# Kernel optimization log

Hardware: AMD Instinct MI355X
Metric: run time of the kernel (lower is better)

The kernel has to match this reference:

```python
import jax, jax.numpy as jnp
import numpy as np

D_MODEL = 1024
D_INNER = 4096
K = 127
B, L = 2, 4096

def setup_inputs() -> dict:
    key = jax.random.key(0)
    k1, k2, k3, k4, k5 = jax.random.split(key, 5)
    x = jax.random.normal(k1, (B, L, D_MODEL), dtype=jnp.float32)
    # in_proj: Linear(d, 2*m) -> weight [2m, d] (torch convention)
    w_in = jax.random.normal(k2, (2 * D_INNER, D_MODEL), dtype=jnp.float32) * (1.0 / np.sqrt(D_MODEL))
    # depthwise conv weight: [m, 1, k] in torch; store as [m, k]
    w_dw = jax.random.normal(k3, (D_INNER, K), dtype=jnp.float32) * (1.0 / np.sqrt(K))
    b_dw = jax.random.normal(k4, (D_INNER,), dtype=jnp.float32) * 0.01
    # out_proj: Linear(m, d) -> weight [d, m]
    w_out = jax.random.normal(k5, (D_MODEL, D_INNER), dtype=jnp.float32) * (1.0 / np.sqrt(D_INNER))
    return {"x": x, "w_in": w_in, "w_dw": w_dw, "b_dw": b_dw, "w_out": w_out}

def _causal_dwconv(v, w_dw, b_dw):
    # v: [B, L, m]; causal depthwise conv with kernel K
    # pad K-1 on the left only (equivalent to torch pad=K-1 then [..., :L])
    v_bcl = jnp.transpose(v, (0, 2, 1))  # [B, m, L]
    out = jax.lax.conv_general_dilated(
        v_bcl,
        w_dw[:, None, :],  # [m, 1, K]
        window_strides=(1,),
        padding=[(K - 1, 0)],
        feature_group_count=D_INNER,
        dimension_numbers=("NCH", "OIH", "NCH"),
    )
    out = out + b_dw[None, :, None]
    return jnp.transpose(out, (0, 2, 1))  # [B, L, m]

def reference(x, w_in, w_dw, b_dw, w_out):
    vg = jnp.einsum("bld,ed->ble", x, w_in)  # [B, L, 2m]
    v, g = jnp.split(vg, 2, axis=-1)
    v = _causal_dwconv(v, w_dw, b_dw)
    y = jax.nn.silu(v) * jax.nn.silu(g)
    return jnp.einsum("blm,dm->bld", y, w_out)
```

## Files before the change

kernel.cpp:

```cpp
#include <hip/hip_runtime.h>
#include <hip/hip_bf16.h>
#include <cstdint>
#include <cstddef>

typedef __fp16 f16_t;
typedef __attribute__((ext_vector_type(8))) __fp16 f16x8;
typedef __attribute__((ext_vector_type(4))) __fp16 f16x4;
typedef __attribute__((ext_vector_type(2))) __fp16 h2_t;
typedef __attribute__((ext_vector_type(4))) float floatx4;

__device__ __forceinline__ void async_copy_16B(const void* g, void* l) {
  __builtin_amdgcn_global_load_lds(
      (const __attribute__((address_space(1))) void*)g,
      (__attribute__((address_space(3))) void*)l, 16, 0, 0);
}

__global__ __launch_bounds__(256) void prep(
    const float* __restrict__ x, const float* __restrict__ w_in,
    const float* __restrict__ w_out, const float* __restrict__ w_dw,
    f16_t* __restrict__ x_h, f16_t* __restrict__ wi_h,
    f16_t* __restrict__ wo_h, h2_t* __restrict__ wp) {
  const int tid = blockIdx.x * 256 + threadIdx.x;
  if (tid < 5242880) {
    const float* src;
    f16_t* dst;
    int off;
    if (tid < 2097152) {
      src = x; dst = x_h; off = tid;
    } else if (tid < 4194304) {
      src = w_in; dst = wi_h; off = tid - 2097152;
    } else {
      src = w_out; dst = wo_h; off = tid - 4194304;
    }
    const float4 v = *(const float4*)(src + (size_t)off * 4);
    f16x4 o;
    o.x = (f16_t)v.x; o.y = (f16_t)v.y; o.z = (f16_t)v.z; o.w = (f16_t)v.w;
    *(f16x4*)(dst + (size_t)off * 4) = o;
  } else {
    const int idx = tid - 5242880;
    if (idx < 128 * 4096) {
      const int p = idx >> 12;
      const int c = idx & 4095;
      float a, b;
      if (p < 126) {
        a = w_dw[c * 127 + p]; b = w_dw[c * 127 + p + 1];
      } else if (p == 126) {
        a = w_dw[c * 127 + 126]; b = 0.f;
      } else {
        a = 0.f; b = w_dw[c * 127 + 0];
      }
      h2_t w;
      w.x = (f16_t)a; w.y = (f16_t)b;
      wp[idx] = w;
    }
  }
}

__global__ __launch_bounds__(512, 2) void gemm256_d4(
    const f16_t* __restrict__ A, const f16_t* __restrict__ B,
    f16_t* __restrict__ C, int M, int N, int K) {
  extern __shared__ char smem[];
  const int t = threadIdx.x;
  const int lane = t & 63;
  const int wave = t >> 6;
  const int wm = wave >> 2;
  const int wn = wave & 3;

  const int bid = blockIdx.x;
  const int xcd = bid & 7;
  const int l = bid >> 3;
  const int quad = l >> 5;
  const int qm = (l >> 3) & 3;
  const int qn = l & 7;
  const int m0 = ((xcd >> 1) * 8 + (quad >> 1) * 4 + qm) * 256;
  const int n0 = ((xcd & 1) * 16 + (quad & 1) * 8 + qn) * 256;

  auto stageTile = [&](int bf_, int k0) {
    char* base = smem + bf_ * 32768;
#pragma unroll
    for (int u = 0; u < 2; ++u) {
      const int q = u * 512 + t;
      const int row = ((q >> 6) << 4) + (q & 15);
      const int g = (q >> 4) & 3;
      async_copy_16B(A + (size_t)(m0 + row) * K + k0 + g * 8, base + q * 16);
    }
#pragma unroll
    for (int u = 0; u < 2; ++u) {
      const int q = u * 512 + t;
      const int row = ((q >> 6) << 4) + (q & 15);
      const int g = (q >> 4) & 3;
      async_copy_16B(B + (size_t)(n0 + row) * K + k0 + g * 8,
                     base + 16384 + q * 16);
    }
  };
  auto ldA = [&](int bf_, int blk) -> f16x8 {
    return *(const f16x8*)(smem + bf_ * 32768 + blk * 1024 + lane * 16);
  };
  auto ldB = [&](int bf_, int blk) -> f16x8 {
    return *(const f16x8*)(smem + bf_ * 32768 + 16384 + blk * 1024 +
                           lane * 16);
  };

  floatx4 acc[8][4] = {};
  const int kT = K / 32;

  stageTile(0, 0);
  stageTile(1, 32);
  stageTile(2, 64);
  for (int tt = 0; tt < kT; ++tt) {
    const int bf_ = tt & 3;
    const int rem = kT - 1 - tt;
    if (rem >= 3) {
      stageTile((tt + 3) & 3, (tt + 3) * 32);
      asm volatile("s_waitcnt vmcnt(12)" ::: "memory");
    } else if (rem == 2) {
      asm volatile("s_waitcnt vmcnt(8)" ::: "memory");
    } else if (rem == 1) {
      asm volatile("s_waitcnt vmcnt(4)" ::: "memory");
    } else {
      asm volatile("s_waitcnt vmcnt(0)" ::: "memory");
    }
    __builtin_amdgcn_s_barrier();

    f16x8 bfr[4];
#pragma unroll
    for (int j = 0; j < 4; ++j) bfr[j] = ldB(bf_, wn * 4 + j);
    __builtin_amdgcn_s_setprio(1);
#pragma unroll
    for (int ii = 0; ii < 8; ++ii) {
      const f16x8 af = ldA(bf_, wm * 8 + ii);
#pragma unroll
      for (int j = 0; j < 4; ++j)
        acc[ii][j] = __builtin_amdgcn_mfma_f32_16x16x32_f16(
            af, bfr[j], acc[ii][j], 0, 0, 0);
    }
    __builtin_amdgcn_s_setprio(0);
    __builtin_amdgcn_s_barrier();
  }

  const int cr = (lane >> 4) * 4;
  const int cc = lane & 15;
#pragma unroll
  for (int i = 0; i < 8; ++i)
#pragma unroll
    for (int j = 0; j < 4; ++j)
#pragma unroll
      for (int r = 0; r < 4; ++r) {
        const int row = m0 + wm * 128 + i * 16 + cr + r;
        const int col = n0 + wn * 64 + j * 16 + cc;
        C[(size_t)row * N + col] = (f16_t)acc[i][j][r];
      }
}

__global__ __launch_bounds__(512, 2) void gemmN128_d3(
    const f16_t* __restrict__ A, const f16_t* __restrict__ B,
    float* __restrict__ C, int M, int N, int K) {
  extern __shared__ char smem[];
  const int t = threadIdx.x;
  const int lane = t & 63;
  const int wave = t >> 6;
  const int wm = wave >> 2;
  const int wn = wave & 3;

  const int bid = blockIdx.x;
  const int xcd = bid & 7;
  const int l = bid >> 3;
  const int m0 = (xcd * 4 + (l >> 3)) * 256;
  const int n0 = (l & 7) * 128;

  auto stageTile = [&](int bf_, int k0) {
    char* base = smem + bf_ * 49152;
#pragma unroll
    for (int u = 0; u < 4; ++u) {
      const int q = u * 512 + t;
      const int frag = q >> 6;
      const int row = (frag >> 1) * 16 + (q & 15);
      const int col = (frag & 1) * 32 + ((q >> 4) & 3) * 8;
      async_copy_16B(A + (size_t)(m0 + row) * K + k0 + col, base + q * 16);
    }
#pragma unroll
    for (int u = 0; u < 2; ++u) {
      const int q = u * 512 + t;
      const int frag = q >> 6;
      const int row = (frag >> 1) * 16 + (q & 15);
      const int col = (frag & 1) * 32 + ((q >> 4) & 3) * 8;
      async_copy_16B(B + (size_t)(n0 + row) * K + k0 + col,
                     base + 32768 + q * 16);
    }
  };
  auto ldA = [&](int bf_, int frag) -> f16x8 {
    return *(const f16x8*)(smem + bf_ * 49152 + frag * 1024 + lane * 16);
  };
  auto ldB = [&](int bf_, int frag) -> f16x8 {
    return *(const f16x8*)(smem + bf_ * 49152 + 32768 + frag * 1024 +
                           lane * 16);
  };

  floatx4 acc[8][2] = {};
  const int kT = K / 64;

  stageTile(0, 0);
  stageTile(1, 64);
  for (int tt = 0; tt < kT; ++tt) {
    const int bf_ = tt % 3;
    const int rem = kT - 1 - tt;
    if (rem >= 2) {
      stageTile((tt + 2) % 3, (tt + 2) * 64);
      asm volatile("s_waitcnt vmcnt(12)" ::: "memory");
    } else if (rem == 1) {
      asm volatile("s_waitcnt vmcnt(6)" ::: "memory");
    } else {
      asm volatile("s_waitcnt vmcnt(0)" ::: "memory");
    }
    __builtin_amdgcn_s_barrier();

    f16x8 bfr[2][2];
#pragma unroll
    for (int j = 0; j < 2; ++j)
#pragma unroll
      for (int kh = 0; kh < 2; ++kh)
        bfr[j][kh] = ldB(bf_, (wn * 2 + j) * 2 + kh);
    __builtin_amdgcn_s_setprio(1);
#pragma unroll
    for (int ii = 0; ii < 8; ++ii) {
      const f16x8 af0 = ldA(bf_, (wm * 8 + ii) * 2 + 0);
      const f16x8 af1 = ldA(bf_, (wm * 8 + ii) * 2 + 1);
#pragma unroll
      for (int j = 0; j < 2; ++j)
        acc[ii][j] = __builtin_amdgcn_mfma_f32_16x16x32_f16(
            af0, bfr[j][0], acc[ii][j], 0, 0, 0);
#pragma unroll
      for (int j = 0; j < 2; ++j)
        acc[ii][j] = __builtin_amdgcn_mfma_f32_16x16x32_f16(
            af1, bfr[j][1], acc[ii][j], 0, 0, 0);
    }
    __builtin_amdgcn_s_setprio(0);
    __builtin_amdgcn_s_barrier();
  }

  const int cr = (lane >> 4) * 4;
  const int cc = lane & 15;
#pragma unroll
  for (int i = 0; i < 8; ++i)
#pragma unroll
    for (int j = 0; j < 2; ++j)
#pragma unroll
      for (int r = 0; r < 4; ++r) {
        const int row = m0 + wm * 128 + i * 16 + cr + r;
        const int col = n0 + wn * 32 + j * 16 + cc;
        C[(size_t)row * N + col] = acc[i][j][r];
      }
}

#define CONV_L 128
#define CPAIRS 127

__global__ __launch_bounds__(256) void conv_gate(
    const f16_t* __restrict__ vg, const h2_t* __restrict__ wp,
    const float* __restrict__ b_dw, f16_t* __restrict__ y) {
  __shared__ uint32_t vtp[CPAIRS * 64];
  __shared__ uint32_t wpl[128 * 64];
  const int t = threadIdx.x;
  const int lane = t & 63;
  const int wave = t >> 6;
  const int c0 = blockIdx.x * 64;
  const int lt = blockIdx.y & 31;
  const int b = blockIdx.y >> 5;
  const int l0 = lt * CONV_L;

#pragma unroll
  for (int it = 0; it < 8; ++it) {
    const int q = it * 256 + t;
    async_copy_16B(wp + (size_t)(q >> 4) * 4096 + c0 + (q & 15) * 4,
                   wpl + q * 4);
  }
  for (int q = t; q < CPAIRS * 8; q += 256) {
    const int m = q >> 3;
    const int oc = (q & 7) * 8;
    const int le = l0 - 126 + 2 * m;
    uint4 a = make_uint4(0u, 0u, 0u, 0u);
    uint4 bb = make_uint4(0u, 0u, 0u, 0u);
    if (le >= 0) {
      const size_t base = (size_t)(b * 4096 + le) * 8192 + c0 + oc;
      a = *(const uint4*)(vg + base);
      bb = *(const uint4*)(vg + base + 8192);
    }
    uint32_t* dst = vtp + m * 64 + oc;
    const uint32_t aw[4] = {a.x, a.y, a.z, a.w};
    const uint32_t bw[4] = {bb.x, bb.y, bb.z, bb.w};
#pragma unroll
    for (int i = 0; i < 4; ++i) {
      dst[2 * i] = (aw[i] & 0xFFFFu) | (bw[i] << 16);
      dst[2 * i + 1] = (aw[i] >> 16) | (bw[i] & 0xFFFF0000u);
    }
  }

  const int c = c0 + lane;
  const int lb = l0 + wave * 32;
  const f16_t* gp = vg + (size_t)(b * 4096 + lb) * 8192 + 4096 + c;
  f16_t gvals[32];
#pragma unroll
  for (int i = 0; i < 32; ++i) gvals[i] = gp[(size_t)i * 8192];

  __syncthreads();

  const float bias = b_dw[c];
  float acc[32];
#pragma unroll
  for (int i = 0; i < 32; ++i) acc[i] = bias;

  const uint32_t* vbase = vtp + wave * 16 * 64 + lane;
  const uint32_t* wbase = wpl + lane;

  h2_t ring[17];
#pragma unroll
  for (int m = 0; m < 17; ++m)
    ring[m] = __builtin_bit_cast(h2_t, vbase[m * 64]);

  {
    const h2_t w0 = __builtin_bit_cast(h2_t, wbase[127 * 64]);
#pragma unroll
    for (int h = 0; h < 16; ++h)
      acc[2 * h + 1] =
          __builtin_amdgcn_fdot2(w0, ring[h], acc[2 * h + 1], false);
  }

#pragma unroll
  for (int k = 0; k < 64; ++k) {
    const h2_t we = __builtin_bit_cast(h2_t, wbase[(2 * k) * 64]);
#pragma unroll
    for (int h = 0; h < 16; ++h)
      acc[2 * h] =
          __builtin_amdgcn_fdot2(we, ring[(k + h) % 17], acc[2 * h], false);
    if (k < 63) {
      const h2_t wo = __builtin_bit_cast(h2_t, wbase[(2 * k + 1) * 64]);
#pragma unroll
      for (int h = 0; h < 16; ++h)
        acc[2 * h + 1] = __builtin_amdgcn_fdot2(wo, ring[(k + 1 + h) % 17],
                                                acc[2 * h + 1], false);
      if (k < 62)
        ring[k % 17] = __builtin_bit_cast(h2_t, vbase[(17 + k) * 64]);
    }
  }

  f16_t* yp = y + (size_t)(b * 4096 + lb) * 4096 + c;
#pragma unroll
  for (int i = 0; i < 32; ++i) {
    const float gv = (float)gvals[i];
    const float v = acc[i];
    const float sv = v / (1.f + __expf(-v));
    const float sg = gv / (1.f + __expf(-gv));
    yp[(size_t)i * 4096] = (f16_t)(sv * sg);
  }
}

extern "C" void kernel_launch(void* const* d_in, const int* in_sizes, int n_in,
                              void* d_out, int out_size, void* d_ws,
                              size_t ws_size, hipStream_t stream) {
  const float* x     = (const float*)d_in[0];
  const float* w_in  = (const float*)d_in[1];
  const float* w_dw  = (const float*)d_in[2];
  const float* b_dw  = (const float*)d_in[3];
  const float* w_out = (const float*)d_in[4];
  float* out = (float*)d_out;

  char* p = (char*)d_ws;
  f16_t* x_h  = (f16_t*)p; p += (size_t)8192 * 1024 * 2;
  f16_t* wi_h = (f16_t*)p; p += (size_t)8192 * 1024 * 2;
  f16_t* wo_h = (f16_t*)p; p += (size_t)1024 * 4096 * 2;
  h2_t*  wp   = (h2_t*)p;  p += (size_t)128 * 4096 * 4;
  f16_t* vg   = (f16_t*)p; p += (size_t)8192 * 8192 * 2;
  f16_t* y    = (f16_t*)p; p += (size_t)8192 * 4096 * 2;

  prep<<<22528, 256, 0, stream>>>(x, w_in, w_out, w_dw, x_h, wi_h, wo_h, wp);

  hipFuncSetAttribute(reinterpret_cast<const void*>(gemm256_d4),
                      hipFuncAttributeMaxDynamicSharedMemorySize, 131072);
  gemm256_d4<<<1024, 512, 131072, stream>>>(x_h, wi_h, vg, 8192, 8192, 1024);

  conv_gate<<<dim3(64, 64), 256, 0, stream>>>(vg, wp, b_dw, y);

  hipFuncSetAttribute(reinterpret_cast<const void*>(gemmN128_d3),
                      hipFuncAttributeMaxDynamicSharedMemorySize, 147456);
  gemmN128_d3<<<256, 512, 147456, stream>>>(y, wo_h, out, 8192, 1024, 4096);
}
```

Baseline: 485.2 us.

## Replace both GEMMs with a shared 128x128 double-buffered templated kernel

Both projection GEMMs now use one templated kernel with 128x128 tiles, 256 threads, a 2-stage LDS buffer (32KB) and launch bounds allowing 4 blocks per CU. This replaces the 256x256 4-stage and 256x128 3-stage kernels. The aim is more resident blocks and latency hiding through thread-level parallelism instead of deep prefetch. In exchange, each tile reuses its operands less, global/L2 traffic goes up, and the shallower pipeline may expose load latency.

```diff
diff --git a/kernel.cpp b/kernel.cpp
--- a/kernel.cpp
+++ b/kernel.cpp
@@ -56,66 +56,71 @@
   }
 }
 
-__global__ __launch_bounds__(512, 2) void gemm256_d4(
+template <typename OutT, int GMODE>
+__global__ __launch_bounds__(256, 4) void gemm_tlp(
     const f16_t* __restrict__ A, const f16_t* __restrict__ B,
-    f16_t* __restrict__ C, int M, int N, int K) {
+    OutT* __restrict__ C, int M, int N, int K) {
   extern __shared__ char smem[];
   const int t = threadIdx.x;
   const int lane = t & 63;
   const int wave = t >> 6;
-  const int wm = wave >> 2;
-  const int wn = wave & 3;
-
-  const int bid = blockIdx.x;
-  const int xcd = bid & 7;
-  const int l = bid >> 3;
-  const int quad = l >> 5;
-  const int qm = (l >> 3) & 3;
-  const int qn = l & 7;
-  const int m0 = ((xcd >> 1) * 8 + (quad >> 1) * 4 + qm) * 256;
-  const int n0 = ((xcd & 1) * 16 + (quad & 1) * 8 + qn) * 256;
-
-  auto stageTile = [&](int bf_, int k0) {
-    char* base = smem + bf_ * 32768;
+  const int wm = wave >> 1;
+  const int wn = wave & 1;
+
+  int m0, n0;
+  if (GMODE == 0) {
+    const int bid = blockIdx.x;
+    const int xcd = bid & 7;
+    const int l = bid >> 3;
+    const int q2 = l >> 7;
+    const int im = (l >> 4) & 7;
+    const int in_ = l & 15;
+    const int lm = (q2 >> 1) * 8 + im;
+    const int ln = (q2 & 1) * 16 + in_;
+    m0 = ((xcd >> 1) * 16 + lm) * 128;
+    n0 = ((xcd & 1) * 32 + ln) * 128;
+  } else {
+    const int bid = blockIdx.x;
+    const int xcd = bid & 7;
+    const int l = bid >> 3;
+    m0 = (xcd * 8 + (l >> 3)) * 128;
+    n0 = (l & 7) * 128;
+  }
+
+  auto stageTile = [&](int d, int k0) {
+    char* base = smem + d * 16384;
 #pragma unroll
     for (int u = 0; u < 2; ++u) {
-      const int q = u * 512 + t;
+      const int q = u * 256 + t;
       const int row = ((q >> 6) << 4) + (q & 15);
       const int g = (q >> 4) & 3;
       async_copy_16B(A + (size_t)(m0 + row) * K + k0 + g * 8, base + q * 16);
     }
 #pragma unroll
     for (int u = 0; u < 2; ++u) {
-      const int q = u * 512 + t;
+      const int q = u * 256 + t;
       const int row = ((q >> 6) << 4) + (q & 15);
       const int g = (q >> 4) & 3;
       async_copy_16B(B + (size_t)(n0 + row) * K + k0 + g * 8,
-                     base + 16384 + q * 16);
+                     base + 8192 + q * 16);
     }
   };
-  auto ldA = [&](int bf_, int blk) -> f16x8 {
-    return *(const f16x8*)(smem + bf_ * 32768 + blk * 1024 + lane * 16);
+  auto ldA = [&](int d, int frag) -> f16x8 {
+    return *(const f16x8*)(smem + d * 16384 + frag * 1024 + lane * 16);
   };
-  auto ldB = [&](int bf_, int blk) -> f16x8 {
-    return *(const f16x8*)(smem + bf_ * 32768 + 16384 + blk * 1024 +
+  auto ldB = [&](int d, int frag) -> f16x8 {
+    return *(const f16x8*)(smem + d * 16384 + 8192 + frag * 1024 +
                            lane * 16);
   };
 
-  floatx4 acc[8][4] = {};
+  floatx4 acc[4][4] = {};
   const int kT = K / 32;
 
   stageTile(0, 0);
-  stageTile(1, 32);
-  stageTile(2, 64);
   for (int tt = 0; tt < kT; ++tt) {
-    const int bf_ = tt & 3;
-    const int rem = kT - 1 - tt;
-    if (rem >= 3) {
-      stageTile((tt + 3) & 3, (tt + 3) * 32);
-      asm volatile("s_waitcnt vmcnt(12)" ::: "memory");
-    } else if (rem == 2) {
-      asm volatile("s_waitcnt vmcnt(8)" ::: "memory");
-    } else if (rem == 1) {
+    const int d = tt & 1;
+    if (tt + 1 < kT) {
+      stageTile(d ^ 1, (tt + 1) * 32);
       asm volatile("s_waitcnt vmcnt(4)" ::: "memory");
     } else {
       asm volatile("s_waitcnt vmcnt(0)" ::: "memory");
@@ -124,15 +129,15 @@
 
     f16x8 bfr[4];
 #pragma unroll
-    for (int j = 0; j < 4; ++j) bfr[j] = ldB(bf_, wn * 4 + j);
+    for (int j = 0; j < 4; ++j) bfr[j] = ldB(d, wn * 4 + j);
     __builtin_amdgcn_s_setprio(1);
 #pragma unroll
-    for (int ii = 0; ii < 8; ++ii) {
-      const f16x8 af = ldA(bf_, wm * 8 + ii);
+    for (int i = 0; i < 4; ++i) {
+      const f16x8 af = ldA(d, wm * 4 + i);
 #pragma unroll
       for (int j = 0; j < 4; ++j)
-        acc[ii][j] = __builtin_amdgcn_mfma_f32_16x16x32_f16(
-            af, bfr[j], acc[ii][j], 0, 0, 0);
+        acc[i][j] = __builtin_amdgcn_mfma_f32_16x16x32_f16(
+            af, bfr[j], acc[i][j], 0, 0, 0);
     }
     __builtin_amdgcn_s_setprio(0);
     __builtin_amdgcn_s_barrier();
@@ -141,114 +146,14 @@
   const int cr = (lane >> 4) * 4;
   const int cc = lane & 15;
 #pragma unroll
-  for (int i = 0; i < 8; ++i)
+  for (int i = 0; i < 4; ++i)
 #pragma unroll
     for (int j = 0; j < 4; ++j)
 #pragma unroll
       for (int r = 0; r < 4; ++r) {
-        const int row = m0 + wm * 128 + i * 16 + cr + r;
+        const int row = m0 + wm * 64 + i * 16 + cr + r;
         const int col = n0 + wn * 64 + j * 16 + cc;
-        C[(size_t)row * N + col] = (f16_t)acc[i][j][r];
-      }
-}
-
-__global__ __launch_bounds__(512, 2) void gemmN128_d3(
-    const f16_t* __restrict__ A, const f16_t* __restrict__ B,
-    float* __restrict__ C, int M, int N, int K) {
-  extern __shared__ char smem[];
-  const int t = threadIdx.x;
-  const int lane = t & 63;
-  const int wave = t >> 6;
-  const int wm = wave >> 2;
-  const int wn = wave & 3;
-
-  const int bid = blockIdx.x;
-  const int xcd = bid & 7;
-  const int l = bid >> 3;
-  const int m0 = (xcd * 4 + (l >> 3)) * 256;
-  const int n0 = (l & 7) * 128;
-
-  auto stageTile = [&](int bf_, int k0) {
-    char* base = smem + bf_ * 49152;
-#pragma unroll
-    for (int u = 0; u < 4; ++u) {
-      const int q = u * 512 + t;
-      const int frag = q >> 6;
-      const int row = (frag >> 1) * 16 + (q & 15);
-      const int col = (frag & 1) * 32 + ((q >> 4) & 3) * 8;
-      async_copy_16B(A + (size_t)(m0 + row) * K + k0 + col, base + q * 16);
-    }
-#pragma unroll
-    for (int u = 0; u < 2; ++u) {
-      const int q = u * 512 + t;
-      const int frag = q >> 6;
-      const int row = (frag >> 1) * 16 + (q & 15);
-      const int col = (frag & 1) * 32 + ((q >> 4) & 3) * 8;
-      async_copy_16B(B + (size_t)(n0 + row) * K + k0 + col,
-                     base + 32768 + q * 16);
-    }
-  };
-  auto ldA = [&](int bf_, int frag) -> f16x8 {
-    return *(const f16x8*)(smem + bf_ * 49152 + frag * 1024 + lane * 16);
-  };
-  auto ldB = [&](int bf_, int frag) -> f16x8 {
-    return *(const f16x8*)(smem + bf_ * 49152 + 32768 + frag * 1024 +
-                           lane * 16);
-  };
-
-  floatx4 acc[8][2] = {};
-  const int kT = K / 64;
-
-  stageTile(0, 0);
-  stageTile(1, 64);
-  for (int tt = 0; tt < kT; ++tt) {
-    const int bf_ = tt % 3;
-    const int rem = kT - 1 - tt;
-    if (rem >= 2) {
-      stageTile((tt + 2) % 3, (tt + 2) * 64);
-      asm volatile("s_waitcnt vmcnt(12)" ::: "memory");
-    } else if (rem == 1) {
-      asm volatile("s_waitcnt vmcnt(6)" ::: "memory");
-    } else {
-      asm volatile("s_waitcnt vmcnt(0)" ::: "memory");
-    }
-    __builtin_amdgcn_s_barrier();
-
-    f16x8 bfr[2][2];
-#pragma unroll
-    for (int j = 0; j < 2; ++j)
-#pragma unroll
-      for (int kh = 0; kh < 2; ++kh)
-        bfr[j][kh] = ldB(bf_, (wn * 2 + j) * 2 + kh);
-    __builtin_amdgcn_s_setprio(1);
-#pragma unroll
-    for (int ii = 0; ii < 8; ++ii) {
-      const f16x8 af0 = ldA(bf_, (wm * 8 + ii) * 2 + 0);
-      const f16x8 af1 = ldA(bf_, (wm * 8 + ii) * 2 + 1);
-#pragma unroll
-      for (int j = 0; j < 2; ++j)
-        acc[ii][j] = __builtin_amdgcn_mfma_f32_16x16x32_f16(
-            af0, bfr[j][0], acc[ii][j], 0, 0, 0);
-#pragma unroll
-      for (int j = 0; j < 2; ++j)
-        acc[ii][j] = __builtin_amdgcn_mfma_f32_16x16x32_f16(
-            af1, bfr[j][1], acc[ii][j], 0, 0, 0);
-    }
-    __builtin_amdgcn_s_setprio(0);
-    __builtin_amdgcn_s_barrier();
-  }
-
-  const int cr = (lane >> 4) * 4;
-  const int cc = lane & 15;
-#pragma unroll
-  for (int i = 0; i < 8; ++i)
-#pragma unroll
-    for (int j = 0; j < 2; ++j)
-#pragma unroll
-      for (int r = 0; r < 4; ++r) {
-        const int row = m0 + wm * 128 + i * 16 + cr + r;
-        const int col = n0 + wn * 32 + j * 16 + cc;
-        C[(size_t)row * N + col] = acc[i][j][r];
+        C[(size_t)row * N + col] = (OutT)acc[i][j][r];
       }
 }
 
@@ -374,13 +279,15 @@
 
   prep<<<22528, 256, 0, stream>>>(x, w_in, w_out, w_dw, x_h, wi_h, wo_h, wp);
 
-  hipFuncSetAttribute(reinterpret_cast<const void*>(gemm256_d4),
-                      hipFuncAttributeMaxDynamicSharedMemorySize, 131072);
-  gemm256_d4<<<1024, 512, 131072, stream>>>(x_h, wi_h, vg, 8192, 8192, 1024);
+  hipFuncSetAttribute((const void*)gemm_tlp<f16_t, 0>,
+                      hipFuncAttributeMaxDynamicSharedMemorySize, 32768);
+  gemm_tlp<f16_t, 0><<<4096, 256, 32768, stream>>>(x_h, wi_h, vg,
+                                                   8192, 8192, 1024);
 
   conv_gate<<<dim3(64, 64), 256, 0, stream>>>(vg, wp, b_dw, y);
 
-  hipFuncSetAttribute(reinterpret_cast<const void*>(gemmN128_d3),
-                      hipFuncAttributeMaxDynamicSharedMemorySize, 147456);
-  gemmN128_d3<<<256, 512, 147456, stream>>>(y, wo_h, out, 8192, 1024, 4096);
-}
+  hipFuncSetAttribute((const void*)gemm_tlp<float, 1>,
+                      hipFuncAttributeMaxDynamicSharedMemorySize, 32768);
+  gemm_tlp<float, 1><<<512, 256, 32768, stream>>>(y, wo_h, out,
+                                                  8192, 1024, 4096);
+}
```

Measured after the change: 607.2 us. +25.1%, slower.
